# Kernel tuning notes

Hardware: AMD Instinct MI355X
Metric: run time of the kernel (lower is better)

Reference implementation:

```python
import jax, jax.numpy as jnp
import numpy as np


def _bilinear_sample(img, gx, gy):
    # img: [B,C,H,W]; gx,gy: [B,N] normalized coords in [-1,1]
    # Matches torch F.grid_sample(mode='bilinear', padding_mode='border', align_corners=False)
    B, C, H, W = img.shape
    ix = ((gx + 1.0) * W - 1.0) * 0.5
    iy = ((gy + 1.0) * H - 1.0) * 0.5
    ix = jnp.clip(ix, 0.0, W - 1.0)  # border padding: clip source coords
    iy = jnp.clip(iy, 0.0, H - 1.0)
    x0 = jnp.floor(ix); y0 = jnp.floor(iy)
    wx = ix - x0; wy = iy - y0
    x0i = x0.astype(jnp.int32); y0i = y0.astype(jnp.int32)
    x1i = jnp.minimum(x0i + 1, W - 1); y1i = jnp.minimum(y0i + 1, H - 1)
    imt = jnp.transpose(img, (0, 2, 3, 1))  # [B,H,W,C]
    b = jnp.arange(B)[:, None]
    v00 = imt[b, y0i, x0i]  # [B,N,C]
    v01 = imt[b, y0i, x1i]
    v10 = imt[b, y1i, x0i]
    v11 = imt[b, y1i, x1i]
    w00 = ((1 - wy) * (1 - wx))[..., None]
    w01 = ((1 - wy) * wx)[..., None]
    w10 = (wy * (1 - wx))[..., None]
    w11 = (wy * wx)[..., None]
    out = v00 * w00 + v01 * w01 + v10 * w10 + v11 * w11  # [B,N,C]
    return jnp.transpose(out, (0, 2, 1))  # [B,C,N]


def _conv1x1(W, b, x):
    # W: [Cout,Cin], b: [Cout], x: [B,Cin,N] -> [B,Cout,N]
    return jnp.einsum('oc,bcn->bon', W, x) + b[None, :, None]


def setup_inputs() -> dict:
    key = jax.random.key(0)
    ks = jax.random.split(key, 12)
    B, N = 4, 65536
    C_FEAT = 64
    CH = [67, 128, 128]
    x_loc = jax.random.uniform(ks[0], (B, 3, N), dtype=jnp.float32)
    x_feat = jax.random.normal(ks[1], (B, C_FEAT, N), dtype=jnp.float32)
    m0 = jax.random.normal(ks[2], (B, 64, 128, 128), dtype=jnp.float32)
    m1 = jax.random.normal(ks[3], (B, 128, 128, 128), dtype=jnp.float32)
    m2 = jax.random.normal(ks[4], (B, 256, 128, 128), dtype=jnp.float32)
    # SharedMLP params (kaiming-ish scale)
    W1 = jax.random.normal(ks[5], (CH[1], CH[0]), dtype=jnp.float32) * (1.0 / np.sqrt(CH[0]))
    b1 = jnp.zeros((CH[1],), dtype=jnp.float32)
    W2 = jax.random.normal(ks[6], (CH[2], CH[1]), dtype=jnp.float32) * (1.0 / np.sqrt(CH[1]))
    b2 = jnp.zeros((CH[2],), dtype=jnp.float32)
    # resid_loc: zero-init except identity on first two input channels (x/y of x_loc)
    Wr = jnp.zeros((2, CH[2] + 3), dtype=jnp.float32).at[0, 0].set(1.0).at[1, 1].set(1.0)
    br = jnp.zeros((2,), dtype=jnp.float32)
    return dict(x_loc=x_loc, x_feat=x_feat, m0=m0, m1=m1, m2=m2,
                W1=W1, b1=b1, W2=W2, b2=b2, Wr=Wr, br=br)


def reference(x_loc, x_feat, m0, m1, m2, W1, b1, W2, b2, Wr, br):
    # loc = Sequential(SharedMLP([67,128,128]), ReLU)
    h = jnp.concatenate([x_loc, x_feat], axis=1)          # [B,67,N]
    h = jax.nn.relu(_conv1x1(W1, b1, h))                  # [B,128,N]
    h = jax.nn.relu(_conv1x1(W2, b2, h))                  # [B,128,N]
    h = jnp.concatenate([x_loc, h], axis=1)               # [B,131,N]
    grid = _conv1x1(Wr, br, h)                            # [B,2,N]
    gx, gy = grid[:, 0, :], grid[:, 1, :]                 # grid last dim = (x, y)
    pooled = [_bilinear_sample(m, gx, gy) for m in (m0, m1, m2)]
    return jnp.concatenate(pooled, axis=1)                # [B,448,N]
```

## Files before the change

### kernel.cpp

```cpp
#include <hip/hip_runtime.h>
#include <hip/hip_bf16.h>

typedef __bf16 bf16x8 __attribute__((ext_vector_type(8)));
typedef __bf16 bf16x4 __attribute__((ext_vector_type(4)));
typedef float  f32x4  __attribute__((ext_vector_type(4)));

#define N_PTS  65536
#define B_SZ   4
#define P_TOT  (B_SZ * N_PTS)
#define PITCH1 104
#define PITCH2 136

__global__ __launch_bounds__(256) void mlp_grid_kernel(
    const float* __restrict__ x_loc, const float* __restrict__ x_feat,
    const float* __restrict__ W1, const float* __restrict__ b1,
    const float* __restrict__ W2, const float* __restrict__ b2,
    const float* __restrict__ Wr, const float* __restrict__ br,
    float* __restrict__ grid_out)
{
    __shared__ __bf16 stage[64 * PITCH1];
    __shared__ __bf16 h1s[64 * PITCH2];
    __shared__ float  gpart[16][2][64];

    const int tid = threadIdx.x;
    const int w   = tid >> 6;
    const int l   = tid & 63;
    const int q   = l >> 4;
    const int lp  = l & 15;
    const int pt0 = blockIdx.x * 64;

    bf16x8 w1f[2][3];
    bf16x8 w2f[2][4];
    float  b1v[2][4], b2v[2][4], wrp[2][2][4];
    for (int i = 0; i < 2; ++i) {
        const int o = (2 * w + i) * 16 + lp;
        for (int ks = 0; ks < 3; ++ks) {
            const int k0 = ks * 32 + q * 8;
            bf16x8 a;
            #pragma unroll
            for (int j = 0; j < 8; ++j) {
                const int k = k0 + j;
                const float v = (k < 67) ? W1[o * 67 + k] : 0.0f;
                a[j] = (__bf16)v;
            }
            w1f[i][ks] = a;
        }
        for (int ks = 0; ks < 4; ++ks) {
            const int k0 = ks * 32 + q * 8;
            bf16x8 a;
            #pragma unroll
            for (int j = 0; j < 8; ++j) a[j] = (__bf16)W2[o * 128 + k0 + j];
            w2f[i][ks] = a;
        }
        const int ob = (2 * w + i) * 16 + q * 4;
        #pragma unroll
        for (int r = 0; r < 4; ++r) {
            b1v[i][r]    = b1[ob + r];
            b2v[i][r]    = b2[ob + r];
            wrp[0][i][r] = Wr[0 * 131 + 3 + ob + r];
            wrp[1][i][r] = Wr[1 * 131 + 3 + ob + r];
        }
    }

    {
        const int kk = tid >> 6;
        const int pt = tid & 63;
        const int p  = pt0 + pt;
        const int b  = p >> 16;
        const int n  = p & 0xFFFF;
        for (int kb = 0; kb < 68; kb += 4) {
            const int k = kb + kk;
            if (k < 67) {
                const float v = (k < 3) ? x_loc[((b * 3 + k) << 16) | n]
                                        : x_feat[((b * 64 + (k - 3)) << 16) | n];
                stage[pt * PITCH1 + k] = (__bf16)v;
            }
        }
        for (int k = 67 + kk; k < 96; k += 4) stage[pt * PITCH1 + k] = (__bf16)0.0f;
    }
    __syncthreads();

    for (int col = 0; col < 4; ++col) {
        const int pt = col * 16 + lp;
        bf16x8 bfr[3];
        #pragma unroll
        for (int ks = 0; ks < 3; ++ks)
            bfr[ks] = *(const bf16x8*)&stage[pt * PITCH1 + ks * 32 + q * 8];
        #pragma unroll
        for (int i = 0; i < 2; ++i) {
            f32x4 acc = {0.f, 0.f, 0.f, 0.f};
            #pragma unroll
            for (int ks = 0; ks < 3; ++ks)
                acc = __builtin_amdgcn_mfma_f32_16x16x32_bf16(w1f[i][ks], bfr[ks], acc, 0, 0, 0);
            bf16x4 hv;
            #pragma unroll
            for (int r = 0; r < 4; ++r)
                hv[r] = (__bf16)fmaxf(acc[r] + b1v[i][r], 0.0f);
            *(bf16x4*)&h1s[pt * PITCH2 + (2 * w + i) * 16 + q * 4] = hv;
        }
    }
    __syncthreads();

    for (int col = 0; col < 4; ++col) {
        const int pt = col * 16 + lp;
        bf16x8 bfr[4];
        #pragma unroll
        for (int ks = 0; ks < 4; ++ks)
            bfr[ks] = *(const bf16x8*)&h1s[pt * PITCH2 + ks * 32 + q * 8];
        float p0 = 0.f, p1 = 0.f;
        #pragma unroll
        for (int i = 0; i < 2; ++i) {
            f32x4 acc = {0.f, 0.f, 0.f, 0.f};
            #pragma unroll
            for (int ks = 0; ks < 4; ++ks)
                acc = __builtin_amdgcn_mfma_f32_16x16x32_bf16(w2f[i][ks], bfr[ks], acc, 0, 0, 0);
            #pragma unroll
            for (int r = 0; r < 4; ++r) {
                const float v = fmaxf(acc[r] + b2v[i][r], 0.0f);
                p0 += wrp[0][i][r] * v;
                p1 += wrp[1][i][r] * v;
            }
        }
        gpart[w * 4 + q][0][pt] = p0;
        gpart[w * 4 + q][1][pt] = p1;
    }
    __syncthreads();

    if (tid < 128) {
        const int o  = tid >> 6;
        const int pt = tid & 63;
        const int p  = pt0 + pt;
        const int b  = p >> 16;
        const int n  = p & 0xFFFF;
        float s = br[o];
        #pragma unroll
        for (int c = 0; c < 3; ++c)
            s += Wr[o * 131 + c] * x_loc[((b * 3 + c) << 16) | n];
        #pragma unroll
        for (int g = 0; g < 16; ++g) s += gpart[g][o][pt];
        grid_out[o * P_TOT + p] = s;
    }
}

__global__ __launch_bounds__(1024) void sample_kernel(
    const float* __restrict__ m0, const float* __restrict__ m1,
    const float* __restrict__ m2, const float* __restrict__ grid,
    float* __restrict__ out)
{
    const int p = blockIdx.x * 1024 + threadIdx.x;
    const int b = p >> 16;
    const int n = p & 0xFFFF;
    const float gx = grid[p];
    const float gy = grid[P_TOT + p];

    float ix = ((gx + 1.0f) * 128.0f - 1.0f) * 0.5f;
    float iy = ((gy + 1.0f) * 128.0f - 1.0f) * 0.5f;
    ix = fminf(fmaxf(ix, 0.0f), 127.0f);
    iy = fminf(fmaxf(iy, 0.0f), 127.0f);
    const float x0f = floorf(ix);
    const float y0f = floorf(iy);
    const float wx = ix - x0f;
    const float wy = iy - y0f;
    const int x0 = (int)x0f, y0 = (int)y0f;
    const int x1 = min(x0 + 1, 127);
    const int y1 = min(y0 + 1, 127);
    const int o00 = y0 * 128 + x0;
    const int o01 = y0 * 128 + x1;
    const int o10 = y1 * 128 + x0;
    const int o11 = y1 * 128 + x1;
    const float w00 = (1.f - wy) * (1.f - wx);
    const float w01 = (1.f - wy) * wx;
    const float w10 = wy * (1.f - wx);
    const float w11 = wy * wx;

    const float* s0 = m0 + (size_t)(b * 64)  * 16384;
    const float* s1 = m1 + (size_t)(b * 128) * 16384;
    const float* s2 = m2 + (size_t)(b * 256) * 16384;
    float* op = out + (size_t)(b * 448) * 65536 + n;

    #pragma unroll 4
    for (int c = 0; c < 64; ++c) {
        const float v = w00 * s0[o00] + w01 * s0[o01] + w10 * s0[o10] + w11 * s0[o11];
        __builtin_nontemporal_store(v, op);
        s0 += 16384; op += 65536;
        if ((c & 15) == 15) __syncthreads();
    }
    #pragma unroll 4
    for (int c = 0; c < 128; ++c) {
        const float v = w00 * s1[o00] + w01 * s1[o01] + w10 * s1[o10] + w11 * s1[o11];
        __builtin_nontemporal_store(v, op);
        s1 += 16384; op += 65536;
        if ((c & 15) == 15) __syncthreads();
    }
    #pragma unroll 4
    for (int c = 0; c < 256; ++c) {
        const float v = w00 * s2[o00] + w01 * s2[o01] + w10 * s2[o10] + w11 * s2[o11];
        __builtin_nontemporal_store(v, op);
        s2 += 16384; op += 65536;
        if ((c & 15) == 15) __syncthreads();
    }
}

extern "C" void kernel_launch(void* const* d_in, const int* in_sizes, int n_in,
                              void* d_out, int out_size, void* d_ws, size_t ws_size,
                              hipStream_t stream)
{
    (void)in_sizes; (void)n_in; (void)out_size; (void)ws_size;
    const float* x_loc  = (const float*)d_in[0];
    const float* x_feat = (const float*)d_in[1];
    const float* m0     = (const float*)d_in[2];
    const float* m1     = (const float*)d_in[3];
    const float* m2     = (const float*)d_in[4];
    const float* W1     = (const float*)d_in[5];
    const float* b1     = (const float*)d_in[6];
    const float* W2     = (const float*)d_in[7];
    const float* b2     = (const float*)d_in[8];
    const float* Wr     = (const float*)d_in[9];
    const float* br     = (const float*)d_in[10];
    float* out  = (float*)d_out;
    float* grid = (float*)d_ws;

    mlp_grid_kernel<<<dim3(P_TOT / 64), dim3(256), 0, stream>>>(
        x_loc, x_feat, W1, b1, W2, b2, Wr, br, grid);
    sample_kernel<<<dim3(P_TOT / 1024), dim3(1024), 0, stream>>>(
        m0, m1, m2, grid, out);
}
```

Baseline: 1.203 ms.

## Stage bounding row band of feature maps into LDS for bilinear sampling

The sampling kernel finds the min and max source row touched by the block's 1024 points using a wave-shuffle plus block reduction. For each of the 448 channels it then copies that row band into a double-buffered LDS slice with global_load_lds, and performs the four bilinear taps from LDS instead of scattered global gathers. This trades per-point gather latency for bulk row streaming plus a block barrier per channel, and it uses about 128KB of LDS per block. Separately, the MLP kernel converts weights once through shared memory, processes four 64-point tiles per block, and loads the input with float4.

```diff
diff --git a/kernel.cpp b/kernel.cpp
--- a/kernel.cpp
+++ b/kernel.cpp
@@ -10,6 +10,13 @@
 #define P_TOT  (B_SZ * N_PTS)
 #define PITCH1 104
 #define PITCH2 136
+
+__device__ __forceinline__ void gload_lds16(const float* g, float* l) {
+    __builtin_amdgcn_global_load_lds(
+        (const __attribute__((address_space(1))) void*)g,
+        (__attribute__((address_space(3))) void*)l,
+        16, 0, 0);
+}
 
 __global__ __launch_bounds__(256) void mlp_grid_kernel(
     const float* __restrict__ x_loc, const float* __restrict__ x_feat,
@@ -18,40 +25,50 @@
     const float* __restrict__ Wr, const float* __restrict__ br,
     float* __restrict__ grid_out)
 {
-    __shared__ __bf16 stage[64 * PITCH1];
-    __shared__ __bf16 h1s[64 * PITCH2];
-    __shared__ float  gpart[16][2][64];
+    __shared__ __align__(16) union SmemU {
+        __bf16 wbuf[128 * 128];
+        struct {
+            __bf16 stage[64 * PITCH1];
+            __bf16 h1s[64 * PITCH2];
+            float  gpart[16][2][64];
+        } r;
+    } u;
 
     const int tid = threadIdx.x;
     const int w   = tid >> 6;
     const int l   = tid & 63;
     const int q   = l >> 4;
     const int lp  = l & 15;
-    const int pt0 = blockIdx.x * 64;
-
+
+    for (int idx = tid; idx < 128 * 96; idx += 256) {
+        const int o = idx / 96;
+        const int k = idx - o * 96;
+        u.wbuf[idx] = (__bf16)((k < 67) ? W1[o * 67 + k] : 0.0f);
+    }
+    __syncthreads();
     bf16x8 w1f[2][3];
-    bf16x8 w2f[2][4];
-    float  b1v[2][4], b2v[2][4], wrp[2][2][4];
+    #pragma unroll
     for (int i = 0; i < 2; ++i) {
         const int o = (2 * w + i) * 16 + lp;
-        for (int ks = 0; ks < 3; ++ks) {
-            const int k0 = ks * 32 + q * 8;
-            bf16x8 a;
-            #pragma unroll
-            for (int j = 0; j < 8; ++j) {
-                const int k = k0 + j;
-                const float v = (k < 67) ? W1[o * 67 + k] : 0.0f;
-                a[j] = (__bf16)v;
-            }
-            w1f[i][ks] = a;
-        }
-        for (int ks = 0; ks < 4; ++ks) {
-            const int k0 = ks * 32 + q * 8;
-            bf16x8 a;
-            #pragma unroll
-            for (int j = 0; j < 8; ++j) a[j] = (__bf16)W2[o * 128 + k0 + j];
-            w2f[i][ks] = a;
-        }
+        #pragma unroll
+        for (int ks = 0; ks < 3; ++ks)
+            w1f[i][ks] = *(const bf16x8*)&u.wbuf[o * 96 + ks * 32 + q * 8];
+    }
+    __syncthreads();
+    for (int idx = tid; idx < 128 * 128; idx += 256)
+        u.wbuf[idx] = (__bf16)W2[idx];
+    __syncthreads();
+    bf16x8 w2f[2][4];
+    #pragma unroll
+    for (int i = 0; i < 2; ++i) {
+        const int o = (2 * w + i) * 16 + lp;
+        #pragma unroll
+        for (int ks = 0; ks < 4; ++ks)
+            w2f[i][ks] = *(const bf16x8*)&u.wbuf[o * 128 + ks * 32 + q * 8];
+    }
+    float b1v[2][4], b2v[2][4], wrp[2][2][4];
+    #pragma unroll
+    for (int i = 0; i < 2; ++i) {
         const int ob = (2 * w + i) * 16 + q * 4;
         #pragma unroll
         for (int r = 0; r < 4; ++r) {
@@ -61,84 +78,97 @@
             wrp[1][i][r] = Wr[1 * 131 + 3 + ob + r];
         }
     }
-
-    {
-        const int kk = tid >> 6;
-        const int pt = tid & 63;
-        const int p  = pt0 + pt;
-        const int b  = p >> 16;
-        const int n  = p & 0xFFFF;
-        for (int kb = 0; kb < 68; kb += 4) {
-            const int k = kb + kk;
-            if (k < 67) {
-                const float v = (k < 3) ? x_loc[((b * 3 + k) << 16) | n]
-                                        : x_feat[((b * 64 + (k - 3)) << 16) | n];
-                stage[pt * PITCH1 + k] = (__bf16)v;
+    __syncthreads();
+
+    for (int t = 0; t < 4; ++t) {
+        const int pt0 = blockIdx.x * 256 + t * 64;
+
+        {
+            const int g4  = tid & 15;
+            const int kk  = tid >> 4;
+            const int ptg = g4 * 4;
+            const int pp  = pt0 + ptg;
+            const int bb  = pp >> 16;
+            const int nn  = pp & 0xFFFF;
+            for (int k = kk; k < 96; k += 16) {
+                if (k < 67) {
+                    const float4 v = (k < 3)
+                        ? *(const float4*)&x_loc[((bb * 3 + k) << 16) | nn]
+                        : *(const float4*)&x_feat[((bb * 64 + (k - 3)) << 16) | nn];
+                    u.r.stage[(ptg + 0) * PITCH1 + k] = (__bf16)v.x;
+                    u.r.stage[(ptg + 1) * PITCH1 + k] = (__bf16)v.y;
+                    u.r.stage[(ptg + 2) * PITCH1 + k] = (__bf16)v.z;
+                    u.r.stage[(ptg + 3) * PITCH1 + k] = (__bf16)v.w;
+                } else if (k >= 67) {
+                    u.r.stage[(ptg + 0) * PITCH1 + k] = (__bf16)0.0f;
+                    u.r.stage[(ptg + 1) * PITCH1 + k] = (__bf16)0.0f;
+                    u.r.stage[(ptg + 2) * PITCH1 + k] = (__bf16)0.0f;
+                    u.r.stage[(ptg + 3) * PITCH1 + k] = (__bf16)0.0f;
+                }
             }
         }
-        for (int k = 67 + kk; k < 96; k += 4) stage[pt * PITCH1 + k] = (__bf16)0.0f;
-    }
-    __syncthreads();
-
-    for (int col = 0; col < 4; ++col) {
-        const int pt = col * 16 + lp;
-        bf16x8 bfr[3];
-        #pragma unroll
-        for (int ks = 0; ks < 3; ++ks)
-            bfr[ks] = *(const bf16x8*)&stage[pt * PITCH1 + ks * 32 + q * 8];
-        #pragma unroll
-        for (int i = 0; i < 2; ++i) {
-            f32x4 acc = {0.f, 0.f, 0.f, 0.f};
+        __syncthreads();
+
+        for (int col = 0; col < 4; ++col) {
+            const int pt = col * 16 + lp;
+            bf16x8 bfr[3];
             #pragma unroll
             for (int ks = 0; ks < 3; ++ks)
-                acc = __builtin_amdgcn_mfma_f32_16x16x32_bf16(w1f[i][ks], bfr[ks], acc, 0, 0, 0);
-            bf16x4 hv;
-            #pragma unroll
-            for (int r = 0; r < 4; ++r)
-                hv[r] = (__bf16)fmaxf(acc[r] + b1v[i][r], 0.0f);
-            *(bf16x4*)&h1s[pt * PITCH2 + (2 * w + i) * 16 + q * 4] = hv;
-        }
-    }
-    __syncthreads();
-
-    for (int col = 0; col < 4; ++col) {
-        const int pt = col * 16 + lp;
-        bf16x8 bfr[4];
-        #pragma unroll
-        for (int ks = 0; ks < 4; ++ks)
-            bfr[ks] = *(const bf16x8*)&h1s[pt * PITCH2 + ks * 32 + q * 8];
-        float p0 = 0.f, p1 = 0.f;
-        #pragma unroll
-        for (int i = 0; i < 2; ++i) {
-            f32x4 acc = {0.f, 0.f, 0.f, 0.f};
+                bfr[ks] = *(const bf16x8*)&u.r.stage[pt * PITCH1 + ks * 32 + q * 8];
+            #pragma unroll
+            for (int i = 0; i < 2; ++i) {
+                f32x4 acc = {0.f, 0.f, 0.f, 0.f};
+                #pragma unroll
+                for (int ks = 0; ks < 3; ++ks)
+                    acc = __builtin_amdgcn_mfma_f32_16x16x32_bf16(w1f[i][ks], bfr[ks], acc, 0, 0, 0);
+                bf16x4 hv;
+                #pragma unroll
+                for (int r = 0; r < 4; ++r)
+                    hv[r] = (__bf16)fmaxf(acc[r] + b1v[i][r], 0.0f);
+                *(bf16x4*)&u.r.h1s[pt * PITCH2 + (2 * w + i) * 16 + q * 4] = hv;
+            }
+        }
+        __syncthreads();
+
+        for (int col = 0; col < 4; ++col) {
+            const int pt = col * 16 + lp;
+            bf16x8 bfr[4];
             #pragma unroll
             for (int ks = 0; ks < 4; ++ks)
-                acc = __builtin_amdgcn_mfma_f32_16x16x32_bf16(w2f[i][ks], bfr[ks], acc, 0, 0, 0);
-            #pragma unroll
-            for (int r = 0; r < 4; ++r) {
-                const float v = fmaxf(acc[r] + b2v[i][r], 0.0f);
-                p0 += wrp[0][i][r] * v;
-                p1 += wrp[1][i][r] * v;
+                bfr[ks] = *(const bf16x8*)&u.r.h1s[pt * PITCH2 + ks * 32 + q * 8];
+            float p0 = 0.f, p1 = 0.f;
+            #pragma unroll
+            for (int i = 0; i < 2; ++i) {
+                f32x4 acc = {0.f, 0.f, 0.f, 0.f};
+                #pragma unroll
+                for (int ks = 0; ks < 4; ++ks)
+                    acc = __builtin_amdgcn_mfma_f32_16x16x32_bf16(w2f[i][ks], bfr[ks], acc, 0, 0, 0);
+                #pragma unroll
+                for (int r = 0; r < 4; ++r) {
+                    const float v = fmaxf(acc[r] + b2v[i][r], 0.0f);
+                    p0 += wrp[0][i][r] * v;
+                    p1 += wrp[1][i][r] * v;
+                }
             }
-        }
-        gpart[w * 4 + q][0][pt] = p0;
-        gpart[w * 4 + q][1][pt] = p1;
-    }
-    __syncthreads();
-
-    if (tid < 128) {
-        const int o  = tid >> 6;
-        const int pt = tid & 63;
-        const int p  = pt0 + pt;
-        const int b  = p >> 16;
-        const int n  = p & 0xFFFF;
-        float s = br[o];
-        #pragma unroll
-        for (int c = 0; c < 3; ++c)
-            s += Wr[o * 131 + c] * x_loc[((b * 3 + c) << 16) | n];
-        #pragma unroll
-        for (int g = 0; g < 16; ++g) s += gpart[g][o][pt];
-        grid_out[o * P_TOT + p] = s;
+            u.r.gpart[w * 4 + q][0][pt] = p0;
+            u.r.gpart[w * 4 + q][1][pt] = p1;
+        }
+        __syncthreads();
+
+        if (tid < 128) {
+            const int o  = tid >> 6;
+            const int pt = tid & 63;
+            const int pp = pt0 + pt;
+            const int bb = pp >> 16;
+            const int nn = pp & 0xFFFF;
+            float s = br[o];
+            #pragma unroll
+            for (int c = 0; c < 3; ++c)
+                s += Wr[o * 131 + c] * x_loc[((bb * 3 + c) << 16) | nn];
+            #pragma unroll
+            for (int g = 0; g < 16; ++g) s += u.r.gpart[g][o][pt];
+            grid_out[o * P_TOT + pp] = s;
+        }
     }
 }
 
@@ -147,7 +177,13 @@
     const float* __restrict__ m2, const float* __restrict__ grid,
     float* __restrict__ out)
 {
-    const int p = blockIdx.x * 1024 + threadIdx.x;
+    __shared__ float sbuf[2][128 * 128];
+    __shared__ int redmn[16], redmx[16];
+
+    const int tid  = threadIdx.x;
+    const int wv   = tid >> 6;
+    const int lane = tid & 63;
+    const int p = blockIdx.x * 1024 + tid;
     const int b = p >> 16;
     const int n = p & 0xFFFF;
     const float gx = grid[p];
@@ -164,40 +200,57 @@
     const int x0 = (int)x0f, y0 = (int)y0f;
     const int x1 = min(x0 + 1, 127);
     const int y1 = min(y0 + 1, 127);
-    const int o00 = y0 * 128 + x0;
-    const int o01 = y0 * 128 + x1;
-    const int o10 = y1 * 128 + x0;
-    const int o11 = y1 * 128 + x1;
     const float w00 = (1.f - wy) * (1.f - wx);
     const float w01 = (1.f - wy) * wx;
     const float w10 = wy * (1.f - wx);
     const float w11 = wy * wx;
 
-    const float* s0 = m0 + (size_t)(b * 64)  * 16384;
-    const float* s1 = m1 + (size_t)(b * 128) * 16384;
-    const float* s2 = m2 + (size_t)(b * 256) * 16384;
+    int mn = y0, mx = y1;
+    #pragma unroll
+    for (int s = 32; s; s >>= 1) {
+        mn = min(mn, __shfl_xor(mn, s));
+        mx = max(mx, __shfl_xor(mx, s));
+    }
+    if (lane == 0) { redmn[wv] = mn; redmx[wv] = mx; }
+    __syncthreads();
+    #pragma unroll
+    for (int i = 0; i < 16; ++i) { mn = min(mn, redmn[i]); mx = max(mx, redmx[i]); }
+
+    int ymin = mn;
+    int R = mx - mn + 1;
+    if (R & 1) { if (ymin > 0) --ymin; ++R; }
+    const int nchunk = R >> 1;
+
+    const int a00 = (y0 - ymin) * 128 + x0;
+    const int d01 = x1 - x0;
+    const int d10 = (y1 - y0) * 128;
+
+    auto slice = [&](int c) -> const float* {
+        if (c < 64)  return m0 + ((size_t)(b * 64  + c)         << 14);
+        if (c < 192) return m1 + ((size_t)(b * 128 + (c - 64))  << 14);
+        return              m2 + ((size_t)(b * 256 + (c - 192)) << 14);
+    };
+    auto stage = [&](const float* src, int bsel) {
+        const float* g = src + ymin * 128 + (lane << 2);
+        for (int ch = wv; ch < nchunk; ch += 16)
+            gload_lds16(g + (ch << 8), &sbuf[bsel][ch << 8]);
+    };
+
     float* op = out + (size_t)(b * 448) * 65536 + n;
 
-    #pragma unroll 4
-    for (int c = 0; c < 64; ++c) {
-        const float v = w00 * s0[o00] + w01 * s0[o01] + w10 * s0[o10] + w11 * s0[o11];
+    stage(slice(0), 0);
+    for (int c = 0; c < 448; ++c) {
+        const int cur = c & 1;
+        __syncthreads();
+        if (c + 1 < 448) stage(slice(c + 1), cur ^ 1);
+        const float* sb = sbuf[cur];
+        const float v00 = sb[a00];
+        const float v01 = sb[a00 + d01];
+        const float v10 = sb[a00 + d10];
+        const float v11 = sb[a00 + d01 + d10];
+        const float v = w00 * v00 + w01 * v01 + w10 * v10 + w11 * v11;
         __builtin_nontemporal_store(v, op);
-        s0 += 16384; op += 65536;
-        if ((c & 15) == 15) __syncthreads();
-    }
-    #pragma unroll 4
-    for (int c = 0; c < 128; ++c) {
-        const float v = w00 * s1[o00] + w01 * s1[o01] + w10 * s1[o10] + w11 * s1[o11];
-        __builtin_nontemporal_store(v, op);
-        s1 += 16384; op += 65536;
-        if ((c & 15) == 15) __syncthreads();
-    }
-    #pragma unroll 4
-    for (int c = 0; c < 256; ++c) {
-        const float v = w00 * s2[o00] + w01 * s2[o01] + w10 * s2[o10] + w11 * s2[o11];
-        __builtin_nontemporal_store(v, op);
-        s2 += 16384; op += 65536;
-        if ((c & 15) == 15) __syncthreads();
+        op += 65536;
     }
 }
 
@@ -220,7 +273,7 @@
     float* out  = (float*)d_out;
     float* grid = (float*)d_ws;
 
-    mlp_grid_kernel<<<dim3(P_TOT / 64), dim3(256), 0, stream>>>(
+    mlp_grid_kernel<<<dim3(P_TOT / 256), dim3(256), 0, stream>>>(
         x_loc, x_feat, W1, b1, W2, b2, Wr, br, grid);
     sample_kernel<<<dim3(P_TOT / 1024), dim3(1024), 0, stream>>>(
         m0, m1, m2, grid, out);
```

After: 1.131 ms. -6.1%, faster.
